# Kernel tuning notes

Measured on AMD Instinct MI355X. Metric: run time of the kernel, lower is better.

The kernel has to match this reference:

```python
import jax, jax.numpy as jnp
import numpy as np

NEG_INF = -1e30


def setup_inputs() -> dict:
    key = jax.random.key(0)
    k1, k2, k3, k4, k5, k6 = jax.random.split(key, 6)
    B, CL, QL, H = 16, 512, 64, 768
    c = jax.random.normal(k1, (B, CL, H), dtype=jnp.float32)
    q = jax.random.normal(k2, (B, QL, H), dtype=jnp.float32)
    c_mask = jax.random.randint(k3, (B, CL), 0, 2, dtype=jnp.int32)
    q_mask = jax.random.randint(k4, (B, QL), 0, 2, dtype=jnp.int32)
    W = jax.random.normal(k5, (H, H), dtype=jnp.float32) * (1.0 / np.sqrt(H))
    b = jax.random.normal(k6, (H,), dtype=jnp.float32) * 0.01
    return {"c": c, "q": q, "c_mask": c_mask, "q_mask": q_mask, "W": W, "b": b}


def reference(c, q, c_mask, q_mask, W, b):
    # c: [B, CL, H], q: [B, QL, H]
    cm = c_mask.astype(bool)[:, :, None]   # [B, CL, 1]
    qm = q_mask.astype(bool)[:, None, :]   # [B, 1, QL]
    # projected context then similarity matrix s: [B, CL, QL]
    cp = jnp.einsum('bch,dh->bcd', c, W) + b
    s = jnp.einsum('bcd,bqd->bcq', cp, q)
    # dual masked softmax (c2q over query dim, q2c over context dim)
    s1 = jax.nn.softmax(jnp.where(qm, s, NEG_INF), axis=2)  # [B, CL, QL]
    s2 = jax.nn.softmax(jnp.where(cm, s, NEG_INF), axis=1)  # [B, CL, QL]
    # a = s1 @ q : context-to-query attention
    a = jnp.einsum('bcq,bqh->bch', s1, q)
    # bvec = (s1 @ s2^T) @ c : query-to-context attention
    ss = jnp.einsum('bcq,bdq->bcd', s1, s2)  # [B, CL, CL]
    bvec = jnp.einsum('bcd,bdh->bch', ss, c)
    x = jnp.concatenate([c, a, c * a, c * bvec], axis=2)  # [B, CL, 4H]
    return x
```

## Files before the change

kernel.cpp:

```cpp
#include <hip/hip_runtime.h>
#include <math.h>


#define B_  16
#define CL_ 512
#define QL_ 64
#define H_  768
#define M_  (B_ * CL_)

typedef __attribute__((ext_vector_type(8))) short s8v;
typedef __attribute__((ext_vector_type(4))) float f4v;

__device__ __forceinline__ unsigned short bf16_rne(float x) {
    unsigned int u = __float_as_uint(x);
    u += 0x7fffu + ((u >> 16) & 1u);
    return (unsigned short)(u >> 16);
}
__device__ __forceinline__ float bf16_f(unsigned short h) {
    return __uint_as_float((unsigned int)h << 16);
}
__device__ __forceinline__ void split2(float x, unsigned short& h, unsigned short& l) {
    h = bf16_rne(x);
    l = bf16_rne(x - bf16_f(h));
}

__global__ __launch_bounds__(256) void k_u_beta(const float* __restrict__ q,
    const float* __restrict__ W, const float* __restrict__ bias,
    unsigned short* __restrict__ uh, unsigned short* __restrict__ ul,
    float* __restrict__ beta)
{
    if (blockIdx.x >= 192) {
        const int row = (blockIdx.x - 192) * 4 + (threadIdx.x >> 6);
        const int lane = threadIdx.x & 63;
        float p = 0.f;
        for (int d = lane; d < H_; d += 64) p = fmaf(bias[d], q[(size_t)row * H_ + d], p);
#pragma unroll
        for (int o = 32; o; o >>= 1) p += __shfl_xor(p, o);
        if (lane == 0) beta[row] = p;
        return;
    }
    __shared__ unsigned short Wh[64][40], Wl[64][40];
    const int m0 = (blockIdx.x & 15) * 64, n0 = (blockIdx.x >> 4) * 64;
    const int t = threadIdx.x, w = t >> 6, lane = t & 63;
    const int fm = lane & 15, quad = lane >> 4;
    const int mrow = m0 + w * 16 + fm;
    const int dd = t >> 3, hc = (t & 7) * 8;
    f4v acc[4];
#pragma unroll
    for (int j = 0; j < 4; ++j) acc[j] = (f4v){0.f, 0.f, 0.f, 0.f};
    for (int k0 = 0; k0 < H_; k0 += 32) {
        const float* wp = &W[(size_t)(k0 + dd) * H_ + n0 + hc];
        const float4 v0 = *(const float4*)wp, v1 = *(const float4*)(wp + 4);
        const float* ap = &q[(size_t)mrow * H_ + k0 + quad * 8];
        const float4 a0 = *(const float4*)ap, a1 = *(const float4*)(ap + 4);
        const float as[8] = {a0.x, a0.y, a0.z, a0.w, a1.x, a1.y, a1.z, a1.w};
        s8v fah, fal;
#pragma unroll
        for (int j = 0; j < 8; ++j) { unsigned short h, l; split2(as[j], h, l); fah[j] = (short)h; fal[j] = (short)l; }
        const float ws[8] = {v0.x, v0.y, v0.z, v0.w, v1.x, v1.y, v1.z, v1.w};
        __syncthreads();
#pragma unroll
        for (int j = 0; j < 8; ++j) {
            unsigned short h, l; split2(ws[j], h, l);
            Wh[hc + j][dd] = h; Wl[hc + j][dd] = l;
        }
        __syncthreads();
#pragma unroll
        for (int tn = 0; tn < 4; ++tn) {
            const s8v bh = *(const s8v*)&Wh[tn * 16 + fm][quad * 8];
            const s8v bl = *(const s8v*)&Wl[tn * 16 + fm][quad * 8];
            acc[tn] = __builtin_amdgcn_mfma_f32_16x16x32_bf16(fah, bh, acc[tn], 0, 0, 0);
            acc[tn] = __builtin_amdgcn_mfma_f32_16x16x32_bf16(fah, bl, acc[tn], 0, 0, 0);
            acc[tn] = __builtin_amdgcn_mfma_f32_16x16x32_bf16(fal, bh, acc[tn], 0, 0, 0);
        }
    }
#pragma unroll
    for (int tn = 0; tn < 4; ++tn) {
        const int col = n0 + tn * 16 + fm;
#pragma unroll
        for (int r = 0; r < 4; ++r) {
            const int row = m0 + w * 16 + quad * 4 + r;
            unsigned short h, l; split2(acc[tn][r], h, l);
            uh[(size_t)row * H_ + col] = h;
            ul[(size_t)row * H_ + col] = l;
        }
    }
}

__global__ __launch_bounds__(256) void k_s_sm(const float* __restrict__ c,
    const unsigned short* __restrict__ uh, const unsigned short* __restrict__ ul,
    const float* __restrict__ beta, const int* __restrict__ q_mask,
    float* __restrict__ sT, unsigned short* __restrict__ s1)
{
    __shared__ unsigned short chh[2][16][40], cll[2][16][40];
    __shared__ float sL[16][65];
    const int m0 = blockIdx.x * 16;
    const int batch = m0 >> 9;
    const int cloc = m0 & (CL_ - 1);
    const int t = threadIdx.x, w = t >> 6, lane = t & 63;
    const int fm = lane & 15, quad = lane >> 4;
    const int srow = t >> 4, skk = (t & 15) * 2;
    f4v acc = (f4v){0.f, 0.f, 0.f, 0.f};

    float2 v = *(const float2*)&c[(size_t)(m0 + srow) * H_ + skk];
    int p = 0;
    for (int k0 = 0; k0 < H_; k0 += 32) {
        unsigned short h0s, l0s, h1s, l1s;
        split2(v.x, h0s, l0s); split2(v.y, h1s, l1s);
        *(ushort2*)&chh[p][srow][skk] = make_ushort2(h0s, h1s);
        *(ushort2*)&cll[p][srow][skk] = make_ushort2(l0s, l1s);
        __syncthreads();
        if (k0 + 32 < H_) v = *(const float2*)&c[(size_t)(m0 + srow) * H_ + k0 + 32 + skk];
        const s8v fah = *(const s8v*)&chh[p][fm][quad * 8];
        const s8v fal = *(const s8v*)&cll[p][fm][quad * 8];
        const size_t bo = (size_t)(batch * QL_ + w * 16 + fm) * H_ + k0 + quad * 8;
        const s8v bh = *(const s8v*)&uh[bo];
        const s8v bl = *(const s8v*)&ul[bo];
        acc = __builtin_amdgcn_mfma_f32_16x16x32_bf16(fah, bh, acc, 0, 0, 0);
        acc = __builtin_amdgcn_mfma_f32_16x16x32_bf16(fah, bl, acc, 0, 0, 0);
        acc = __builtin_amdgcn_mfma_f32_16x16x32_bf16(fal, bh, acc, 0, 0, 0);
        p ^= 1;
    }
    {
        const int col = w * 16 + fm;
        const float bb = beta[batch * QL_ + col];
#pragma unroll
        for (int r = 0; r < 4; ++r) {
            const int lr = quad * 4 + r;
            sL[lr][col] = acc[r] + bb;
        }
    }
    __syncthreads();
    const bool qm = q_mask[batch * QL_ + lane] != 0;
#pragma unroll
    for (int rr = 0; rr < 4; ++rr) {
        const int lr = w * 4 + rr;
        const float x = qm ? sL[lr][lane] : -1e30f;
        float mx = x;
#pragma unroll
        for (int o = 32; o; o >>= 1) mx = fmaxf(mx, __shfl_xor(mx, o));
        const float e = __expf(x - mx);
        float sm = e;
#pragma unroll
        for (int o = 32; o; o >>= 1) sm += __shfl_xor(sm, o);
        s1[(size_t)(m0 + lr) * QL_ + lane] = bf16_rne(e / sm);
    }
    {
        const int qq = t >> 2, c4o = (t & 3) * 4;
        float4 ov;
        ov.x = sL[c4o + 0][qq];
        ov.y = sL[c4o + 1][qq];
        ov.z = sL[c4o + 2][qq];
        ov.w = sL[c4o + 3][qq];
        *(float4*)&sT[((size_t)batch * QL_ + qq) * CL_ + cloc + c4o] = ov;
    }
}

__global__ __launch_bounds__(512) void k_tfin3(const float* __restrict__ sT,
    const unsigned short* __restrict__ s1, const float* __restrict__ q,
    const float* __restrict__ c, const int* __restrict__ c_mask,
    float* __restrict__ out)
{
    __shared__ unsigned short s2L[64 * 512];
    __shared__ unsigned short Bs[2][2][64][40];
    __shared__ unsigned short qT[64][72];
    __shared__ unsigned short tT[64][72];
    const int h0 = blockIdx.x * 64;
    const int b  = blockIdx.y;
    const int t = threadIdx.x, w = t >> 6, lane = t & 63;
    const int fm = lane & 15, quad = lane >> 4;
    const int grp = w >> 2;
    const int wl  = w & 3;

    {
        const int cbase8 = lane * 8;
        int cm8[8];
#pragma unroll
        for (int j = 0; j < 8; ++j) cm8[j] = c_mask[b * CL_ + cbase8 + j];
        const float* stb = sT + (size_t)b * QL_ * CL_;
#pragma unroll
        for (int qi = 0; qi < 8; ++qi) {
            const int qq = w * 8 + qi;
            const float* sr = stb + (size_t)qq * CL_ + cbase8;
            const float4 v0 = *(const float4*)sr, v1 = *(const float4*)(sr + 4);
            float x[8] = {v0.x, v0.y, v0.z, v0.w, v1.x, v1.y, v1.z, v1.w};
#pragma unroll
            for (int j = 0; j < 8; ++j) x[j] = cm8[j] ? x[j] : -1e30f;
            float m = x[0];
#pragma unroll
            for (int j = 1; j < 8; ++j) m = fmaxf(m, x[j]);
#pragma unroll
            for (int o = 32; o; o >>= 1) m = fmaxf(m, __shfl_xor(m, o));
            float e[8], sm = 0.f;
#pragma unroll
            for (int j = 0; j < 8; ++j) { e[j] = __expf(x[j] - m); sm += e[j]; }
#pragma unroll
            for (int o = 32; o; o >>= 1) sm += __shfl_xor(sm, o);
            const float inv = 1.f / sm;
            s8v sv;
#pragma unroll
            for (int j = 0; j < 8; ++j) sv[j] = (short)bf16_rne(e[j] * inv);
            const int boff = ((qq * 512 + cbase8) * 2) ^ ((qq & 7) << 4);
            *(s8v*)((char*)s2L + boff) = sv;
        }
    }

    {
        const int r = t >> 4, c4 = (t & 15) * 4;
#pragma unroll
        for (int i = 0; i < 2; ++i) {
            const int qr = r + 32 * i;
            const float4 v = *(const float4*)&q[((size_t)b * QL_ + qr) * H_ + h0 + c4];
            qT[c4 + 0][qr] = bf16_rne(v.x);
            qT[c4 + 1][qr] = bf16_rne(v.y);
            qT[c4 + 2][qr] = bf16_rne(v.z);
            qT[c4 + 3][qr] = bf16_rne(v.w);
        }
    }

    f4v acc[4];
#pragma unroll
    for (int j = 0; j < 4; ++j) acc[j] = (f4v){0.f, 0.f, 0.f, 0.f};
    {
        const int tl = t & 255;
        const int dd = tl >> 3, hc = (tl & 7) * 8;
        const int gbase = grp * 256;
        const float* cp0 = &c[((size_t)b * CL_ + gbase + dd) * H_ + h0 + hc];
        float4 v0 = *(const float4*)cp0, v1 = *(const float4*)(cp0 + 4);
        int p = 0;
        for (int d0 = 0; d0 < 256; d0 += 32) {
            const float xs[8] = {v0.x, v0.y, v0.z, v0.w, v1.x, v1.y, v1.z, v1.w};
#pragma unroll
            for (int j = 0; j < 8; ++j) Bs[grp][p][hc + j][dd] = bf16_rne(xs[j]);
            __syncthreads();
            if (d0 + 32 < 256) {
                const float* cp = &c[((size_t)b * CL_ + gbase + d0 + 32 + dd) * H_ + h0 + hc];
                v0 = *(const float4*)cp; v1 = *(const float4*)(cp + 4);
            }
            const s8v fb = *(const s8v*)&Bs[grp][p][wl * 16 + fm][quad * 8];
#pragma unroll
            for (int tm = 0; tm < 4; ++tm) {
                const int boff = (((tm * 16 + fm) * 512 + gbase + d0 + quad * 8) * 2) ^ ((fm & 7) << 4);
                const s8v fa = *(const s8v*)((const char*)s2L + boff);
                acc[tm] = __builtin_amdgcn_mfma_f32_16x16x32_bf16(fa, fb, acc[tm], 0, 0, 0);
            }
            p ^= 1;
        }
    }
    __syncthreads();
    {
        float* dumpf = (float*)s2L;
        if (grp == 1) {
#pragma unroll
            for (int tm = 0; tm < 4; ++tm)
#pragma unroll
                for (int r = 0; r < 4; ++r)
                    dumpf[((wl * 4 + tm) * 4 + r) * 64 + lane] = acc[tm][r];
        }
        __syncthreads();
        if (grp == 0) {
#pragma unroll
            for (int tm = 0; tm < 4; ++tm)
#pragma unroll
                for (int r = 0; r < 4; ++r)
                    tT[wl * 16 + fm][tm * 16 + quad * 4 + r] =
                        bf16_rne(acc[tm][r] + dumpf[((wl * 4 + tm) * 4 + r) * 64 + lane]);
        }
    }
    __syncthreads();

    {
        const int cbase = w * 64;
        f4v aa[4][4], bb[4][4];
#pragma unroll
        for (int i = 0; i < 4; ++i)
#pragma unroll
            for (int j = 0; j < 4; ++j) { aa[i][j] = (f4v){0.f, 0.f, 0.f, 0.f}; bb[i][j] = aa[i][j]; }
#pragma unroll
        for (int ks = 0; ks < 2; ++ks) {
            s8v fa[4], fq[4], ft[4];
#pragma unroll
            for (int tm = 0; tm < 4; ++tm)
                fa[tm] = *(const s8v*)&s1[(size_t)(b * CL_ + cbase + tm * 16 + fm) * QL_ + ks * 32 + quad * 8];
#pragma unroll
            for (int tn = 0; tn < 4; ++tn) {
                fq[tn] = *(const s8v*)&qT[tn * 16 + fm][ks * 32 + quad * 8];
                ft[tn] = *(const s8v*)&tT[tn * 16 + fm][ks * 32 + quad * 8];
            }
#pragma unroll
            for (int tm = 0; tm < 4; ++tm)
#pragma unroll
                for (int tn = 0; tn < 4; ++tn) {
                    aa[tm][tn] = __builtin_amdgcn_mfma_f32_16x16x32_bf16(fa[tm], fq[tn], aa[tm][tn], 0, 0, 0);
                    bb[tm][tn] = __builtin_amdgcn_mfma_f32_16x16x32_bf16(fa[tm], ft[tn], bb[tm][tn], 0, 0, 0);
                }
        }
#pragma unroll
        for (int tm = 0; tm < 4; ++tm)
#pragma unroll
            for (int tn = 0; tn < 4; ++tn) {
                const int h = h0 + tn * 16 + fm;
#pragma unroll
                for (int r = 0; r < 4; ++r) {
                    const int crow = cbase + tm * 16 + quad * 4 + r;
                    const float cv = c[((size_t)b * CL_ + crow) * H_ + h];
                    const float av = aa[tm][tn][r], bv = bb[tm][tn][r];
                    float* ob = out + (size_t)(b * CL_ + crow) * (4 * H_);
                    ob[h]           = cv;
                    ob[H_ + h]      = av;
                    ob[2 * H_ + h]  = cv * av;
                    ob[3 * H_ + h]  = cv * bv;
                }
            }
    }
}

extern "C" void kernel_launch(void* const* d_in, const int* in_sizes, int n_in,
                              void* d_out, int out_size, void* d_ws, size_t ws_size,
                              hipStream_t stream) {
    const float* c      = (const float*)d_in[0];
    const float* q      = (const float*)d_in[1];
    const int*   c_mask = (const int*)d_in[2];
    const int*   q_mask = (const int*)d_in[3];
    const float* W      = (const float*)d_in[4];
    const float* bias   = (const float*)d_in[5];
    float* out = (float*)d_out;

    char* base = (char*)d_ws;
    unsigned short* uh   = (unsigned short*)(base);
    unsigned short* ul   = (unsigned short*)(base + 1572864);
    float*          beta = (float*)(base + 3145728);
    float*          sT   = (float*)(base + 3149824);
    unsigned short* s1   = (unsigned short*)(base + 5246976);

    k_u_beta <<<dim3(192 + 256), dim3(256), 0, stream>>>(q, W, bias, uh, ul, beta);
    k_s_sm   <<<dim3(512),       dim3(256), 0, stream>>>(c, uh, ul, beta, q_mask, sT, s1);
    k_tfin3  <<<dim3(12, 16),    dim3(512), 0, stream>>>(sT, s1, q, c, c_mask, out);
}
```

Before: 197.3 us.

## Enlarge k_s_sm tile to 32 rows with 512 threads and 64-wide K steps

The similarity/softmax kernel now processes 32 context rows per block with 8 waves, instead of 16 rows with 4 waves. Each K iteration covers 64 elements (two MFMA sub-steps), which halves the number of barriers, and each 16-row half shares the same uh/ul query fragments. The aim is more reuse of the projected-query operands and less per-iteration synchronisation overhead. The trade-off is that the grid drops to 256 blocks, so there is less parallelism to hide latency on a large GPU.

```diff
diff --git a/kernel.cpp b/kernel.cpp
--- a/kernel.cpp
+++ b/kernel.cpp
@@ -87,48 +87,52 @@
     }
 }
 
-__global__ __launch_bounds__(256) void k_s_sm(const float* __restrict__ c,
+__global__ __launch_bounds__(512) void k_s_sm(const float* __restrict__ c,
     const unsigned short* __restrict__ uh, const unsigned short* __restrict__ ul,
     const float* __restrict__ beta, const int* __restrict__ q_mask,
     float* __restrict__ sT, unsigned short* __restrict__ s1)
 {
-    __shared__ unsigned short chh[2][16][40], cll[2][16][40];
-    __shared__ float sL[16][65];
-    const int m0 = blockIdx.x * 16;
+    __shared__ unsigned short chh[2][32][72], cll[2][32][72];
+    __shared__ float sL[32][65];
+    const int m0 = blockIdx.x * 32;
     const int batch = m0 >> 9;
     const int cloc = m0 & (CL_ - 1);
     const int t = threadIdx.x, w = t >> 6, lane = t & 63;
     const int fm = lane & 15, quad = lane >> 4;
-    const int srow = t >> 4, skk = (t & 15) * 2;
+    const int msub = (w >> 2) * 16, ntile = (w & 3) * 16;
+    const int srow = t >> 4, sc4 = (t & 15) * 4;
     f4v acc = (f4v){0.f, 0.f, 0.f, 0.f};
 
-    float2 v = *(const float2*)&c[(size_t)(m0 + srow) * H_ + skk];
+    const size_t urow = (size_t)(batch * QL_ + ntile + fm) * H_;
+
+    float4 v = *(const float4*)&c[(size_t)(m0 + srow) * H_ + sc4];
     int p = 0;
-    for (int k0 = 0; k0 < H_; k0 += 32) {
-        unsigned short h0s, l0s, h1s, l1s;
-        split2(v.x, h0s, l0s); split2(v.y, h1s, l1s);
-        *(ushort2*)&chh[p][srow][skk] = make_ushort2(h0s, h1s);
-        *(ushort2*)&cll[p][srow][skk] = make_ushort2(l0s, l1s);
+    for (int k0 = 0; k0 < H_; k0 += 64) {
+        ushort4 hh, ll;
+        split2(v.x, hh.x, ll.x); split2(v.y, hh.y, ll.y);
+        split2(v.z, hh.z, ll.z); split2(v.w, hh.w, ll.w);
+        *(ushort4*)&chh[p][srow][sc4] = hh;
+        *(ushort4*)&cll[p][srow][sc4] = ll;
         __syncthreads();
-        if (k0 + 32 < H_) v = *(const float2*)&c[(size_t)(m0 + srow) * H_ + k0 + 32 + skk];
-        const s8v fah = *(const s8v*)&chh[p][fm][quad * 8];
-        const s8v fal = *(const s8v*)&cll[p][fm][quad * 8];
-        const size_t bo = (size_t)(batch * QL_ + w * 16 + fm) * H_ + k0 + quad * 8;
-        const s8v bh = *(const s8v*)&uh[bo];
-        const s8v bl = *(const s8v*)&ul[bo];
-        acc = __builtin_amdgcn_mfma_f32_16x16x32_bf16(fah, bh, acc, 0, 0, 0);
-        acc = __builtin_amdgcn_mfma_f32_16x16x32_bf16(fah, bl, acc, 0, 0, 0);
-        acc = __builtin_amdgcn_mfma_f32_16x16x32_bf16(fal, bh, acc, 0, 0, 0);
+        if (k0 + 64 < H_) v = *(const float4*)&c[(size_t)(m0 + srow) * H_ + k0 + 64 + sc4];
+#pragma unroll
+        for (int kk = 0; kk < 2; ++kk) {
+            const s8v fah = *(const s8v*)&chh[p][msub + fm][kk * 32 + quad * 8];
+            const s8v fal = *(const s8v*)&cll[p][msub + fm][kk * 32 + quad * 8];
+            const s8v bh = *(const s8v*)&uh[urow + k0 + kk * 32 + quad * 8];
+            const s8v bl = *(const s8v*)&ul[urow + k0 + kk * 32 + quad * 8];
+            acc = __builtin_amdgcn_mfma_f32_16x16x32_bf16(fah, bh, acc, 0, 0, 0);
+            acc = __builtin_amdgcn_mfma_f32_16x16x32_bf16(fah, bl, acc, 0, 0, 0);
+            acc = __builtin_amdgcn_mfma_f32_16x16x32_bf16(fal, bh, acc, 0, 0, 0);
+        }
         p ^= 1;
     }
     {
-        const int col = w * 16 + fm;
+        const int col = ntile + fm;
         const float bb = beta[batch * QL_ + col];
 #pragma unroll
-        for (int r = 0; r < 4; ++r) {
-            const int lr = quad * 4 + r;
-            sL[lr][col] = acc[r] + bb;
-        }
+        for (int r = 0; r < 4; ++r)
+            sL[msub + quad * 4 + r][col] = acc[r] + bb;
     }
     __syncthreads();
     const bool qm = q_mask[batch * QL_ + lane] != 0;
@@ -146,7 +150,7 @@
         s1[(size_t)(m0 + lr) * QL_ + lane] = bf16_rne(e / sm);
     }
     {
-        const int qq = t >> 2, c4o = (t & 3) * 4;
+        const int qq = t >> 3, c4o = (t & 7) * 4;
         float4 ov;
         ov.x = sL[c4o + 0][qq];
         ov.y = sL[c4o + 1][qq];
@@ -334,6 +338,6 @@
     unsigned short* s1   = (unsigned short*)(base + 5246976);
 
     k_u_beta <<<dim3(192 + 256), dim3(256), 0, stream>>>(q, W, bias, uh, ul, beta);
-    k_s_sm   <<<dim3(512),       dim3(256), 0, stream>>>(c, uh, ul, beta, q_mask, sT, s1);
+    k_s_sm   <<<dim3(256),       dim3(512), 0, stream>>>(c, uh, ul, beta, q_mask, sT, s1);
     k_tfin3  <<<dim3(12, 16),    dim3(512), 0, stream>>>(sT, s1, q, c, c_mask, out);
 }
```

Result: faster. 193.1 us (-2.1%).
